# Optimization experiments

Hardware: AMD Instinct MI355X
Metric: run time of the kernel (lower is better)

Reference implementation:

```python
import jax, jax.numpy as jnp
import numpy as np

N = 4096            # number of proposals
C = 6               # classes incl. background
SCORE_TH = 0.05
NMS_TH = 0.3
DET_LIM = 100
IM_MAX = 1023.0     # clip to [0, im_size-1]
BBOX_W = jnp.array([10.0, 10.0, 10.0, 5.0, 5.0, 5.0], dtype=jnp.float32)


def setup_inputs() -> dict:
    key = jax.random.key(0)
    k1, k2, k3, k4 = jax.random.split(key, 4)
    # realistic 3D proposals inside the 1024^3 volume: lo in [0,900), size in [1,101)
    lo = jax.random.uniform(k1, (N, 3), dtype=jnp.float32) * 900.0
    sz = jax.random.uniform(k2, (N, 3), dtype=jnp.float32) * 100.0 + 1.0
    bbox_proposals = jnp.concatenate([jnp.zeros((N, 1), jnp.float32), lo, lo + sz], axis=1)  # [N,7]
    bbox_pred = jax.random.normal(k3, (N, C * 6), dtype=jnp.float32) * 0.1                   # [N,36]
    cls_score = jax.random.normal(k4, (N, C), dtype=jnp.float32)                              # [N,6]
    return {"bbox_proposals": bbox_proposals, "bbox_pred": bbox_pred, "cls_score": cls_score}


def _bbox_transform_clip(boxes, deltas):
    # boxes: [N,6] (x1,y1,z1,x2,y2,z2); deltas: [N, C*6] -> pred_boxes [N,C,6]
    d = deltas.reshape(N, C, 6) / BBOX_W
    sizes = boxes[:, 3:6] - boxes[:, 0:3] + 1.0          # [N,3]
    ctrs = boxes[:, 0:3] + 0.5 * sizes                   # [N,3]
    pred_ctr = d[:, :, :3] * sizes[:, None, :] + ctrs[:, None, :]
    pred_sz = jnp.exp(d[:, :, 3:]) * sizes[:, None, :]
    lo = jnp.clip(pred_ctr - 0.5 * pred_sz, 0.0, IM_MAX)
    hi = jnp.clip(pred_ctr + 0.5 * pred_sz - 1.0, 0.0, IM_MAX)
    return jnp.concatenate([lo, hi], axis=-1)            # [N,C,6]


def _nms_one_class(bj, sj):
    # bj: [N,6], sj: [N] -> scores with suppressed/below-threshold entries zeroed
    valid = sj > SCORE_TH
    order = jnp.argsort(-sj)
    b = bj[order]
    v = valid[order]
    l, h = b[:, :3], b[:, 3:]
    vol = jnp.prod(h - l + 1.0, axis=1)                                  # [N]
    inter = jnp.prod(
        jnp.clip(jnp.minimum(h[:, None, :], h[None, :, :])
                 - jnp.maximum(l[:, None, :], l[None, :, :]) + 1.0, 0.0, None),
        axis=-1)                                                          # [N,N]
    iou = inter / (vol[:, None] + vol[None, :] - inter)
    idx = jnp.arange(N)

    def body(i, keep):
        supp = keep[i] & (iou[i] > NMS_TH) & (idx > i)
        return keep & ~supp

    keep = jax.lax.fori_loop(0, N, body, v)
    keep_orig = jnp.zeros(N, bool).at[order].set(keep)
    return jnp.where(keep_orig, sj, 0.0)


def reference(bbox_proposals, bbox_pred, cls_score):
    scores = jax.nn.softmax(cls_score, axis=1)            # [N,C]
    boxes = bbox_proposals[:, 1:]                          # [N,6]
    pred_boxes = _bbox_transform_clip(boxes, bbox_pred)    # [N,C,6]
    cls_boxes = jnp.transpose(pred_boxes[:, 1:, :], (1, 0, 2))  # [5,N,6] (skip background)
    cls_scores = scores[:, 1:].T                                 # [5,N]
    kept = jax.vmap(_nms_one_class)(cls_boxes, cls_scores)       # [5,N]
    # top-100 detections-per-image limit (fixed-shape: zero out below image_thresh)
    thresh = jax.lax.top_k(kept.reshape(-1), DET_LIM)[0][-1]
    final = jnp.where(kept >= thresh, kept, 0.0)
    # pack boxes + final score: [5, N, 7]
    return jnp.concatenate([cls_boxes, final[:, :, None]], axis=-1)
```

## Files before the change

kernel.cpp:

```cpp
#include <hip/hip_runtime.h>
#include <stdint.h>

#define NN 4096
#define NCLS 5
#define NWORD 64
#define SCORE_TH 0.05f
#define NMS_TH 0.3f

__device__ __forceinline__ uint32_t fmap(float f) {
    uint32_t u = __float_as_uint(f);
    return (u & 0x80000000u) ? ~u : (u | 0x80000000u);
}
__device__ __forceinline__ float funmap(uint32_t m) {
    uint32_t u = (m & 0x80000000u) ? (m & 0x7fffffffu) : ~m;
    return __uint_as_float(u);
}

__device__ __forceinline__ void gload_lds16(const void* g, void* l) {
    __builtin_amdgcn_global_load_lds(
        (const __attribute__((address_space(1))) uint32_t*)g,
        (__attribute__((address_space(3))) uint32_t*)l, 16, 0, 0);
}

__global__ void k_prep(const float* __restrict__ prop, const float* __restrict__ pred,
                       const float* __restrict__ cls, float* __restrict__ out,
                       uint64_t* __restrict__ skey) {
    int i = blockIdx.x * 256 + threadIdx.x;
    if (i >= NN) return;
    const float* pr = prop + i * 7;
    float l0 = pr[1], l1 = pr[2], l2 = pr[3];
    float h0 = pr[4], h1 = pr[5], h2 = pr[6];
    float s0 = h0 - l0 + 1.f, s1 = h1 - l1 + 1.f, s2 = h2 - l2 + 1.f;
    float c0 = l0 + 0.5f * s0, c1 = l1 + 0.5f * s1, c2 = l2 + 0.5f * s2;

    float sc[6];
    float mx = -3.4e38f;
#pragma unroll
    for (int c = 0; c < 6; ++c) { sc[c] = cls[i * 6 + c]; mx = fmaxf(mx, sc[c]); }
    float sum = 0.f;
#pragma unroll
    for (int c = 0; c < 6; ++c) { sc[c] = expf(sc[c] - mx); sum += sc[c]; }
    float inv = 1.f / sum;

#pragma unroll
    for (int c = 1; c < 6; ++c) {
        const float* d = pred + i * 36 + c * 6;
        float dc0 = d[0] / 10.f, dc1 = d[1] / 10.f, dc2 = d[2] / 10.f;
        float ds0 = d[3] / 5.f, ds1 = d[4] / 5.f, ds2 = d[5] / 5.f;
        float pc0 = dc0 * s0 + c0, pc1 = dc1 * s1 + c1, pc2 = dc2 * s2 + c2;
        float ps0 = expf(ds0) * s0, ps1 = expf(ds1) * s1, ps2 = expf(ds2) * s2;
        float o0 = fminf(fmaxf(pc0 - 0.5f * ps0, 0.f), 1023.f);
        float o1 = fminf(fmaxf(pc1 - 0.5f * ps1, 0.f), 1023.f);
        float o2 = fminf(fmaxf(pc2 - 0.5f * ps2, 0.f), 1023.f);
        float o3 = fminf(fmaxf(pc0 + 0.5f * ps0 - 1.f, 0.f), 1023.f);
        float o4 = fminf(fmaxf(pc1 + 0.5f * ps1 - 1.f, 0.f), 1023.f);
        float o5 = fminf(fmaxf(pc2 + 0.5f * ps2 - 1.f, 0.f), 1023.f);
        float* ob = out + ((size_t)(c - 1) * NN + i) * 7;
        ob[0] = o0; ob[1] = o1; ob[2] = o2; ob[3] = o3; ob[4] = o4; ob[5] = o5;
        float score = sc[c] * inv;
        skey[(c - 1) * NN + i] = ((uint64_t)fmap(score) << 12) | (uint32_t)(4095 - i);
    }
}

__global__ void __launch_bounds__(256) k_sort(const uint64_t* __restrict__ skey,
                                              const float* __restrict__ out,
                                              float* __restrict__ sscores,
                                              unsigned short* __restrict__ order,
                                              float* __restrict__ sboxes) {
    int c = blockIdx.y;
    int i = blockIdx.x * 256 + threadIdx.x;
    const uint64_t* K = skey + c * NN;
    uint64_t ki = K[i];
    int rank = 0;
#pragma unroll 2
    for (int j = 0; j < NN; j += 8) {
        uint64_t k0 = K[j], k1 = K[j + 1], k2 = K[j + 2], k3 = K[j + 3];
        uint64_t k4 = K[j + 4], k5 = K[j + 5], k6 = K[j + 6], k7 = K[j + 7];
        int a = (k0 > ki) + (k1 > ki) + (k2 > ki) + (k3 > ki);
        int b = (k4 > ki) + (k5 > ki) + (k6 > ki) + (k7 > ki);
        rank += a + b;
    }
    int io = c * NN + rank;
    order[io] = (unsigned short)i;
    sscores[io] = funmap((uint32_t)(ki >> 12));
    const float* b = out + ((size_t)c * NN + i) * 7;
    float* sb = sboxes + (size_t)io * 6;
#pragma unroll
    for (int k = 0; k < 6; ++k) sb[k] = b[k];
}

__global__ void __launch_bounds__(256) k_mask(const float* __restrict__ sboxes,
                                              uint64_t* __restrict__ mask,
                                              uint64_t* __restrict__ diag) {
    int tid = threadIdx.x;
    int wid = tid >> 6, lane = tid & 63;
    int rb = blockIdx.y, c = blockIdx.z;
    int cb = rb + blockIdx.x * 4 + wid;
    bool active = (cb < 64);

    __shared__ float cB[4][64][6];
    __shared__ float cV[4][64];

    int r = rb * 64 + lane;
    float rl0 = 0, rl1 = 0, rl2 = 0, rh0 = 0, rh1 = 0, rh2 = 0, vi = 0;
    if (active) {
        const float* rp = sboxes + ((size_t)c * NN + r) * 6;
        rl0 = rp[0]; rl1 = rp[1]; rl2 = rp[2];
        rh0 = rp[3]; rh1 = rp[4]; rh2 = rp[5];
        vi = (rh0 - rl0 + 1.f) * (rh1 - rl1 + 1.f) * (rh2 - rl2 + 1.f);
        const float* cp = sboxes + ((size_t)c * NN + cb * 64 + lane) * 6;
#pragma unroll
        for (int k = 0; k < 6; ++k) cB[wid][lane][k] = cp[k];
        cV[wid][lane] = (cB[wid][lane][3] - cB[wid][lane][0] + 1.f) *
                        (cB[wid][lane][4] - cB[wid][lane][1] + 1.f) *
                        (cB[wid][lane][5] - cB[wid][lane][2] + 1.f);
    }
    __syncthreads();
    if (!active) return;

    uint64_t bits = 0;
    for (int j2 = 0; j2 < 64; ++j2) {
        int j = cb * 64 + j2;
        if (j > r) {
            float w0 = fmaxf(fminf(rh0, cB[wid][j2][3]) - fmaxf(rl0, cB[wid][j2][0]) + 1.f, 0.f);
            float w1 = fmaxf(fminf(rh1, cB[wid][j2][4]) - fmaxf(rl1, cB[wid][j2][1]) + 1.f, 0.f);
            float w2 = fmaxf(fminf(rh2, cB[wid][j2][5]) - fmaxf(rl2, cB[wid][j2][2]) + 1.f, 0.f);
            float inter = w0 * w1 * w2;
            float iou = inter / (vi + cV[wid][j2] - inter);
            if (iou > NMS_TH) bits |= 1ull << j2;
        }
    }
    mask[((size_t)c * NN + r) * NWORD + cb] = bits;
    if (cb == rb) diag[(size_t)c * NN + r] = bits;
}

__global__ void __launch_bounds__(64, 1) k_nms(const float* __restrict__ sscores,
                                               const unsigned short* __restrict__ order,
                                               const uint64_t* __restrict__ mask,
                                               const uint64_t* __restrict__ diag,
                                               float* __restrict__ kept) {
    __shared__ __align__(16) uint64_t ltile[2][64 * 64];
    __shared__ __align__(16) uint64_t ldiag[NN];
    __shared__ uint64_t sh[64];

    int c = blockIdx.x;
    int lane = threadIdx.x;
    const uint64_t* M = mask + (size_t)c * NN * NWORD;
    const uint64_t* D = diag + (size_t)c * NN;
    const float* ss = sscores + c * NN;

    {
        const char* g = (const char*)D + lane * 16;
        char* l = (char*)ldiag;
#pragma unroll
        for (int i = 0; i < 32; ++i) gload_lds16(g + i * 1024, l + i * 1024);
    }
    {
        const char* g = (const char*)M + lane * 16;
        char* l = (char*)ltile[0];
#pragma unroll
        for (int i = 0; i < 32; ++i) gload_lds16(g + i * 1024, l + i * 1024);
    }

    uint64_t remv = 0;
    {
        const float4* sl = (const float4*)(ss + lane * 64);
#pragma unroll
        for (int q = 0; q < 16; ++q) {
            float4 v = sl[q];
            if (!(v.x > SCORE_TH)) remv |= 1ull << (q * 4);
            if (!(v.y > SCORE_TH)) remv |= 1ull << (q * 4 + 1);
            if (!(v.z > SCORE_TH)) remv |= 1ull << (q * 4 + 2);
            if (!(v.w > SCORE_TH)) remv |= 1ull << (q * 4 + 3);
        }
    }

    asm volatile("s_waitcnt vmcnt(0)" ::: "memory");
    __builtin_amdgcn_sched_barrier(0);

    int cur = 0;
#pragma unroll 1
    for (int w = 0; w < 64; ++w) {
        if (w < 63) {
            const char* g = (const char*)(M + ((size_t)(w + 1) << 12)) + lane * 16;
            char* l = (char*)ltile[cur ^ 1];
#pragma unroll
            for (int i = 0; i < 32; ++i) gload_lds16(g + i * 1024, l + i * 1024);
        }
        __builtin_amdgcn_sched_barrier(0);

        uint32_t rlo = __builtin_amdgcn_readlane((uint32_t)remv, w);
        uint32_t rhi = __builtin_amdgcn_readlane((uint32_t)(remv >> 32), w);
        uint64_t rw = ((uint64_t)rhi << 32) | rlo;
        uint64_t mydg = ldiag[(w << 6) | lane];
        uint32_t dgl = (uint32_t)mydg, dgh = (uint32_t)(mydg >> 32);
        uint64_t kmask = 0;
#pragma unroll
        for (int b = 0; b < 64; ++b) {
            uint32_t dlo = __builtin_amdgcn_readlane(dgl, b);
            uint32_t dhi = __builtin_amdgcn_readlane(dgh, b);
            uint64_t dg = ((uint64_t)dhi << 32) | dlo;
            if (!((rw >> b) & 1)) { rw |= dg; kmask |= 1ull << b; }
        }

        const uint64_t* T = ltile[cur];
        uint64_t a0 = 0, a1 = 0, a2 = 0, a3 = 0;
#pragma unroll
        for (int b = 0; b < 64; b += 4) {
            uint64_t m0 = T[((b + 0) << 6) | lane];
            uint64_t m1 = T[((b + 1) << 6) | lane];
            uint64_t m2 = T[((b + 2) << 6) | lane];
            uint64_t m3 = T[((b + 3) << 6) | lane];
            uint64_t k0 = 0ull - ((kmask >> (b + 0)) & 1ull);
            uint64_t k1 = 0ull - ((kmask >> (b + 1)) & 1ull);
            uint64_t k2 = 0ull - ((kmask >> (b + 2)) & 1ull);
            uint64_t k3 = 0ull - ((kmask >> (b + 3)) & 1ull);
            a0 |= m0 & k0;
            a1 |= m1 & k1;
            a2 |= m2 & k2;
            a3 |= m3 & k3;
        }
        if (lane >= w) remv |= (a0 | a1) | (a2 | a3);

        asm volatile("s_waitcnt vmcnt(0)" ::: "memory");
        __builtin_amdgcn_sched_barrier(0);
        cur ^= 1;
    }

    sh[lane] = remv;
    __syncthreads();
    const unsigned short* ord = order + c * NN;
    for (int t = 0; t < 64; ++t) {
        int p = t * 64 + lane;
        bool kp = !((sh[t] >> lane) & 1);
        float s = ss[p];
        int oi = ord[p];
        kept[c * NN + oi] = kp ? s : 0.f;
    }
}

__global__ void __launch_bounds__(1024) k_topk_final(const float* __restrict__ kept,
                                                     float* __restrict__ out) {
    int tid = threadIdx.x;
    uint32_t v[20];
#pragma unroll
    for (int k = 0; k < 20; ++k) v[k] = fmap(kept[k * 1024 + tid]);
    __shared__ int red[16];
    __shared__ int tot;
    uint32_t pre = 0;
    for (int bit = 31; bit >= 0; --bit) {
        uint32_t cand = pre | (1u << bit);
        int cnt = 0;
#pragma unroll
        for (int k = 0; k < 20; ++k) cnt += (v[k] >= cand);
#pragma unroll
        for (int off = 32; off; off >>= 1) cnt += __shfl_down(cnt, off, 64);
        if ((tid & 63) == 0) red[tid >> 6] = cnt;
        __syncthreads();
        if (tid == 0) {
            int s = 0;
            for (int q = 0; q < 16; ++q) s += red[q];
            tot = s;
        }
        __syncthreads();
        if (tot >= 100) pre = cand;
    }
#pragma unroll
    for (int k = 0; k < 20; ++k) {
        int idx = k * 1024 + tid;
        int c = idx >> 12;
        int i = idx & (NN - 1);
        out[((size_t)c * NN + i) * 7 + 6] = (v[k] >= pre) ? funmap(v[k]) : 0.f;
    }
}

extern "C" void kernel_launch(void* const* d_in, const int* in_sizes, int n_in,
                              void* d_out, int out_size, void* d_ws, size_t ws_size,
                              hipStream_t stream) {
    const float* prop = (const float*)d_in[0];
    const float* pred = (const float*)d_in[1];
    const float* cls = (const float*)d_in[2];
    float* out = (float*)d_out;

    char* base = (char*)d_ws;
    uint64_t* skey = (uint64_t*)base;
    uint64_t* diag = (uint64_t*)(base + (160ull << 10));
    float* sscores = (float*)(base + (320ull << 10));
    float* kept = (float*)(base + (400ull << 10));
    unsigned short* order = (unsigned short*)(base + (480ull << 10));
    float* sboxes = (float*)(base + (528ull << 10));
    uint64_t* mask = (uint64_t*)(base + (1ull << 20));

    k_prep<<<dim3(16), dim3(256), 0, stream>>>(prop, pred, cls, out, skey);
    k_sort<<<dim3(16, NCLS), dim3(256), 0, stream>>>(skey, out, sscores, order, sboxes);
    k_mask<<<dim3(16, 64, NCLS), dim3(256), 0, stream>>>(sboxes, mask, diag);
    k_nms<<<dim3(NCLS), dim3(64), 0, stream>>>(sscores, order, mask, diag, kept);
    k_topk_final<<<dim3(1), dim3(1024), 0, stream>>>(kept, out);
}
```

Baseline: 481.2 us.

## Stage NMS mask tiles through registers two ahead instead of global_load_lds

Replaces the direct global-to-LDS loads with ordinary vector loads into a 32-entry uint4 register buffer. Each tile is prefetched two iterations ahead and written to LDS one iteration ahead, and the explicit vmcnt(0) wait at the end of each iteration is dropped, so the global load latency can overlap a full iteration of the serial scan. The readlane chain is also split into batches of 16, so scalar reads are issued ahead of the dependent bit loop. In exchange it adds VGPR pressure from 128 extra registers and relies on the compiler inserting the correct waits before the LDS stores.

```diff
diff --git a/kernel.cpp b/kernel.cpp
--- a/kernel.cpp
+++ b/kernel.cpp
@@ -14,12 +14,6 @@
 __device__ __forceinline__ float funmap(uint32_t m) {
     uint32_t u = (m & 0x80000000u) ? (m & 0x7fffffffu) : ~m;
     return __uint_as_float(u);
-}
-
-__device__ __forceinline__ void gload_lds16(const void* g, void* l) {
-    __builtin_amdgcn_global_load_lds(
-        (const __attribute__((address_space(1))) uint32_t*)g,
-        (__attribute__((address_space(3))) uint32_t*)l, 16, 0, 0);
 }
 
 __global__ void k_prep(const float* __restrict__ prop, const float* __restrict__ pred,
@@ -149,18 +143,30 @@
     const uint64_t* D = diag + (size_t)c * NN;
     const float* ss = sscores + c * NN;
 
+    uint4 rg[32];
+
     {
-        const char* g = (const char*)D + lane * 16;
-        char* l = (char*)ldiag;
-#pragma unroll
-        for (int i = 0; i < 32; ++i) gload_lds16(g + i * 1024, l + i * 1024);
+        const uint4* g = (const uint4*)D;
+#pragma unroll
+        for (int i = 0; i < 32; ++i) rg[i] = g[i * 64 + lane];
+        uint4* l = (uint4*)ldiag;
+#pragma unroll
+        for (int i = 0; i < 32; ++i) l[i * 64 + lane] = rg[i];
     }
     {
-        const char* g = (const char*)M + lane * 16;
-        char* l = (char*)ltile[0];
-#pragma unroll
-        for (int i = 0; i < 32; ++i) gload_lds16(g + i * 1024, l + i * 1024);
-    }
+        const uint4* g = (const uint4*)M;
+#pragma unroll
+        for (int i = 0; i < 32; ++i) rg[i] = g[i * 64 + lane];
+        uint4* l = (uint4*)ltile[0];
+#pragma unroll
+        for (int i = 0; i < 32; ++i) l[i * 64 + lane] = rg[i];
+    }
+    {
+        const uint4* g = (const uint4*)(M + (1ull << 12));
+#pragma unroll
+        for (int i = 0; i < 32; ++i) rg[i] = g[i * 64 + lane];
+    }
+    __builtin_amdgcn_sched_barrier(0);
 
     uint64_t remv = 0;
     {
@@ -175,17 +181,18 @@
         }
     }
 
-    asm volatile("s_waitcnt vmcnt(0)" ::: "memory");
-    __builtin_amdgcn_sched_barrier(0);
-
     int cur = 0;
 #pragma unroll 1
     for (int w = 0; w < 64; ++w) {
         if (w < 63) {
-            const char* g = (const char*)(M + ((size_t)(w + 1) << 12)) + lane * 16;
-            char* l = (char*)ltile[cur ^ 1];
-#pragma unroll
-            for (int i = 0; i < 32; ++i) gload_lds16(g + i * 1024, l + i * 1024);
+            uint4* l = (uint4*)ltile[cur ^ 1];
+#pragma unroll
+            for (int i = 0; i < 32; ++i) l[i * 64 + lane] = rg[i];
+        }
+        if (w < 62) {
+            const uint4* g = (const uint4*)(M + ((size_t)(w + 2) << 12));
+#pragma unroll
+            for (int i = 0; i < 32; ++i) rg[i] = g[i * 64 + lane];
         }
         __builtin_amdgcn_sched_barrier(0);
 
@@ -196,11 +203,21 @@
         uint32_t dgl = (uint32_t)mydg, dgh = (uint32_t)(mydg >> 32);
         uint64_t kmask = 0;
 #pragma unroll
-        for (int b = 0; b < 64; ++b) {
-            uint32_t dlo = __builtin_amdgcn_readlane(dgl, b);
-            uint32_t dhi = __builtin_amdgcn_readlane(dgh, b);
-            uint64_t dg = ((uint64_t)dhi << 32) | dlo;
-            if (!((rw >> b) & 1)) { rw |= dg; kmask |= 1ull << b; }
+        for (int sb = 0; sb < 4; ++sb) {
+            uint32_t lo[16], hi[16];
+#pragma unroll
+            for (int b = 0; b < 16; ++b) {
+                lo[b] = __builtin_amdgcn_readlane(dgl, sb * 16 + b);
+                hi[b] = __builtin_amdgcn_readlane(dgh, sb * 16 + b);
+            }
+#pragma unroll
+            for (int b = 0; b < 16; ++b) {
+                int bb = sb * 16 + b;
+                if (!((rw >> bb) & 1)) {
+                    rw |= ((uint64_t)hi[b] << 32) | lo[b];
+                    kmask |= 1ull << bb;
+                }
+            }
         }
 
         const uint64_t* T = ltile[cur];
@@ -222,7 +239,6 @@
         }
         if (lane >= w) remv |= (a0 | a1) | (a2 | a3);
 
-        asm volatile("s_waitcnt vmcnt(0)" ::: "memory");
         __builtin_amdgcn_sched_barrier(0);
         cur ^= 1;
     }
```

Result: slower. 540.9 us (+12.4%).

## Stream NMS mask tiles into registers instead of double-buffered LDS

Applied to the files above, without the earlier changes.

The sequential NMS kernel drops the double-buffered LDS tile filled by async global-to-LDS loads. Each 64-row mask block is now loaded straight into registers in four 16-row chunks, and those loads are interleaved with the serial readlane suppression chain so memory latency overlaps the dependent bit logic. The diagonal preload also switches to plain vector loads followed by LDS stores. This removes the LDS round trip and the full vmcnt waits, but the next block is no longer prefetched across iterations, which may expose global load latency at the start of each iteration and raises register pressure.

```diff
diff --git a/kernel.cpp b/kernel.cpp
--- a/kernel.cpp
+++ b/kernel.cpp
@@ -14,12 +14,6 @@
 __device__ __forceinline__ float funmap(uint32_t m) {
     uint32_t u = (m & 0x80000000u) ? (m & 0x7fffffffu) : ~m;
     return __uint_as_float(u);
-}
-
-__device__ __forceinline__ void gload_lds16(const void* g, void* l) {
-    __builtin_amdgcn_global_load_lds(
-        (const __attribute__((address_space(1))) uint32_t*)g,
-        (__attribute__((address_space(3))) uint32_t*)l, 16, 0, 0);
 }
 
 __global__ void k_prep(const float* __restrict__ prop, const float* __restrict__ pred,
@@ -139,7 +133,6 @@
                                                const uint64_t* __restrict__ mask,
                                                const uint64_t* __restrict__ diag,
                                                float* __restrict__ kept) {
-    __shared__ __align__(16) uint64_t ltile[2][64 * 64];
     __shared__ __align__(16) uint64_t ldiag[NN];
     __shared__ uint64_t sh[64];
 
@@ -150,16 +143,19 @@
     const float* ss = sscores + c * NN;
 
     {
-        const char* g = (const char*)D + lane * 16;
-        char* l = (char*)ldiag;
-#pragma unroll
-        for (int i = 0; i < 32; ++i) gload_lds16(g + i * 1024, l + i * 1024);
-    }
-    {
-        const char* g = (const char*)M + lane * 16;
-        char* l = (char*)ltile[0];
-#pragma unroll
-        for (int i = 0; i < 32; ++i) gload_lds16(g + i * 1024, l + i * 1024);
+        const uint4* g = (const uint4*)D;
+        uint4* l = (uint4*)ldiag;
+#pragma unroll 1
+        for (int i = 0; i < 32; i += 8) {
+            uint4 t0 = g[(i + 0) * 64 + lane], t1 = g[(i + 1) * 64 + lane];
+            uint4 t2 = g[(i + 2) * 64 + lane], t3 = g[(i + 3) * 64 + lane];
+            uint4 t4 = g[(i + 4) * 64 + lane], t5 = g[(i + 5) * 64 + lane];
+            uint4 t6 = g[(i + 6) * 64 + lane], t7 = g[(i + 7) * 64 + lane];
+            l[(i + 0) * 64 + lane] = t0; l[(i + 1) * 64 + lane] = t1;
+            l[(i + 2) * 64 + lane] = t2; l[(i + 3) * 64 + lane] = t3;
+            l[(i + 4) * 64 + lane] = t4; l[(i + 5) * 64 + lane] = t5;
+            l[(i + 6) * 64 + lane] = t6; l[(i + 7) * 64 + lane] = t7;
+        }
     }
 
     uint64_t remv = 0;
@@ -174,19 +170,42 @@
             if (!(v.w > SCORE_TH)) remv |= 1ull << (q * 4 + 3);
         }
     }
-
-    asm volatile("s_waitcnt vmcnt(0)" ::: "memory");
-    __builtin_amdgcn_sched_barrier(0);
-
-    int cur = 0;
+    __builtin_amdgcn_s_barrier();
+
+#define ISSUE16(buf, base)                                          \
+    _Pragma("unroll") for (int i_ = 0; i_ < 16; ++i_) {             \
+        buf[i_] = R[(((base) + i_) << 6) | lane];                   \
+    }
+
+#define CHAIN16(base)                                               \
+    {                                                               \
+        uint32_t lo_[16], hi_[16];                                  \
+        _Pragma("unroll") for (int b_ = 0; b_ < 16; ++b_) {         \
+            lo_[b_] = __builtin_amdgcn_readlane(dgl, (base) + b_);  \
+            hi_[b_] = __builtin_amdgcn_readlane(dgh, (base) + b_);  \
+        }                                                           \
+        _Pragma("unroll") for (int b_ = 0; b_ < 16; ++b_) {         \
+            int bb_ = (base) + b_;                                  \
+            if (!((rw >> bb_) & 1)) {                               \
+                rw |= ((uint64_t)hi_[b_] << 32) | lo_[b_];          \
+                kmask |= 1ull << bb_;                               \
+            }                                                       \
+        }                                                           \
+    }
+
+#define CONSUME16(buf, base, acc)                                   \
+    _Pragma("unroll") for (int i_ = 0; i_ < 16; ++i_) {             \
+        uint64_t kb_ = 0ull - ((kmask >> ((base) + i_)) & 1ull);    \
+        acc |= buf[i_] & kb_;                                       \
+    }
+
 #pragma unroll 1
     for (int w = 0; w < 64; ++w) {
-        if (w < 63) {
-            const char* g = (const char*)(M + ((size_t)(w + 1) << 12)) + lane * 16;
-            char* l = (char*)ltile[cur ^ 1];
-#pragma unroll
-            for (int i = 0; i < 32; ++i) gload_lds16(g + i * 1024, l + i * 1024);
-        }
+        const uint64_t* R = M + ((size_t)w << 12);
+        uint64_t gA[16], gB[16];
+
+        ISSUE16(gA, 0)
+        ISSUE16(gB, 16)
         __builtin_amdgcn_sched_barrier(0);
 
         uint32_t rlo = __builtin_amdgcn_readlane((uint32_t)remv, w);
@@ -195,37 +214,25 @@
         uint64_t mydg = ldiag[(w << 6) | lane];
         uint32_t dgl = (uint32_t)mydg, dgh = (uint32_t)(mydg >> 32);
         uint64_t kmask = 0;
-#pragma unroll
-        for (int b = 0; b < 64; ++b) {
-            uint32_t dlo = __builtin_amdgcn_readlane(dgl, b);
-            uint32_t dhi = __builtin_amdgcn_readlane(dgh, b);
-            uint64_t dg = ((uint64_t)dhi << 32) | dlo;
-            if (!((rw >> b) & 1)) { rw |= dg; kmask |= 1ull << b; }
-        }
-
-        const uint64_t* T = ltile[cur];
         uint64_t a0 = 0, a1 = 0, a2 = 0, a3 = 0;
-#pragma unroll
-        for (int b = 0; b < 64; b += 4) {
-            uint64_t m0 = T[((b + 0) << 6) | lane];
-            uint64_t m1 = T[((b + 1) << 6) | lane];
-            uint64_t m2 = T[((b + 2) << 6) | lane];
-            uint64_t m3 = T[((b + 3) << 6) | lane];
-            uint64_t k0 = 0ull - ((kmask >> (b + 0)) & 1ull);
-            uint64_t k1 = 0ull - ((kmask >> (b + 1)) & 1ull);
-            uint64_t k2 = 0ull - ((kmask >> (b + 2)) & 1ull);
-            uint64_t k3 = 0ull - ((kmask >> (b + 3)) & 1ull);
-            a0 |= m0 & k0;
-            a1 |= m1 & k1;
-            a2 |= m2 & k2;
-            a3 |= m3 & k3;
-        }
+
+        CHAIN16(0)
+        CONSUME16(gA, 0, a0)
+        ISSUE16(gA, 32)
+        CHAIN16(16)
+        CONSUME16(gB, 16, a1)
+        ISSUE16(gB, 48)
+        CHAIN16(32)
+        CONSUME16(gA, 32, a2)
+        CHAIN16(48)
+        CONSUME16(gB, 48, a3)
+
         if (lane >= w) remv |= (a0 | a1) | (a2 | a3);
-
-        asm volatile("s_waitcnt vmcnt(0)" ::: "memory");
-        __builtin_amdgcn_sched_barrier(0);
-        cur ^= 1;
-    }
+    }
+
+#undef ISSUE16
+#undef CHAIN16
+#undef CONSUME16
 
     sh[lane] = remv;
     __syncthreads();
```

Measured after the change: 411.6 us. 1.17x faster.
